# Performance work log

Hardware: AMD Instinct MI355X
Metric: run time of the kernel (lower is better)

Reference implementation:

```python
import jax, jax.numpy as jnp
import numpy as np

NUM_EXPERTS = 4


def _conv1x1(w, b, x):
    # w: [out,in], b: [out], x: [B,in,H,W]
    return jnp.einsum('oc,bchw->bohw', w, x) + b[None, :, None, None]


def _sobel(x):
    c = x.shape[1]
    kx = jnp.array([[-1., 0., 1.], [-2., 0., 2.], [-1., 0., 1.]], dtype=x.dtype)
    ky = jnp.array([[-1., -2., -1.], [0., 0., 0.], [1., 2., 1.]], dtype=x.dtype)
    wx = jnp.broadcast_to(kx[None, None], (c, 1, 3, 3))
    wy = jnp.broadcast_to(ky[None, None], (c, 1, 3, 3))
    dn = ('NCHW', 'OIHW', 'NCHW')
    gx = jax.lax.conv_general_dilated(x, wx, (1, 1), [(1, 1), (1, 1)],
                                      dimension_numbers=dn, feature_group_count=c)
    gy = jax.lax.conv_general_dilated(x, wy, (1, 1), [(1, 1), (1, 1)],
                                      dimension_numbers=dn, feature_group_count=c)
    return gx, gy


def _bilinear_sample(x, gx, gy):
    # torch F.grid_sample(mode='bilinear', padding_mode='zeros', align_corners=False)
    # x: [B,C,H,W]; gx, gy: [B,Hs,Ws] normalized coords in [-1,1]
    B, C, H, W = x.shape
    ix = ((gx + 1.0) * W - 1.0) * 0.5
    iy = ((gy + 1.0) * H - 1.0) * 0.5
    x0 = jnp.floor(ix)
    y0 = jnp.floor(iy)
    wx1 = ix - x0
    wx0 = 1.0 - wx1
    wy1 = iy - y0
    wy0 = 1.0 - wy1
    xf = x.reshape(B, C, H * W)

    def gather(xc, yc):
        valid = (xc >= 0) & (xc <= W - 1) & (yc >= 0) & (yc <= H - 1)
        xi = jnp.clip(xc, 0, W - 1).astype(jnp.int32)
        yi = jnp.clip(yc, 0, H - 1).astype(jnp.int32)
        idx = yi * W + xi  # [B,Hs,Ws]
        v = jax.vmap(lambda xb, ib: xb[:, ib])(xf, idx)  # [B,C,Hs,Ws]
        return v * valid[:, None].astype(x.dtype)

    return (gather(x0, y0) * (wx0 * wy0)[:, None]
            + gather(x0 + 1, y0) * (wx1 * wy0)[:, None]
            + gather(x0, y0 + 1) * (wx0 * wy1)[:, None]
            + gather(x0 + 1, y0 + 1) * (wx1 * wy1)[:, None])


def _forward(x, wc_e, we_e, wb1, bb1, wb2, bb2, wr, br, wo, bo, wcv, bcv, scale, scale2):
    B, c, h, w = x.shape
    sh = round(h * scale)
    sw = round(w * scale2)

    grad_x, grad_y = _sobel(x)

    # relative-offset coordinate embedding, [1,4,sh,sw]
    ih = (jnp.arange(sh, dtype=x.dtype) + 0.5) / scale
    coor_h = ih - jnp.floor(ih + 0.001) - 0.5  # [sh]
    iw = (jnp.arange(sw, dtype=x.dtype) + 0.5) / scale2
    coor_w = iw - jnp.floor(iw + 0.001) - 0.5  # [sw]
    inp = jnp.stack([
        jnp.full((sh, sw), 1.0 / scale2, dtype=x.dtype),
        jnp.full((sh, sw), 1.0 / scale, dtype=x.dtype),
        jnp.broadcast_to(coor_h[:, None], (sh, sw)),
        jnp.broadcast_to(coor_w[None, :], (sh, sw)),
    ], axis=0)[None]

    emb = jax.nn.relu(_conv1x1(wb2, bb2, jax.nn.relu(_conv1x1(wb1, bb1, inp))))
    offset = _conv1x1(wo, bo, emb)                 # [1,2,sh,sw]
    routing = jax.nn.sigmoid(_conv1x1(wr, br, emb))  # [1,E,sh,sw]

    # per-pixel soft mixture of expert compress/expand matrices
    rw = routing.reshape(NUM_EXPERTS, sh * sw).T   # [N,E]
    wc = (rw @ wc_e.reshape(NUM_EXPERTS, -1)).reshape(sh, sw, c // 8, c)
    we = (rw @ we_e.reshape(NUM_EXPERTS, -1)).reshape(sh, sw, c, c // 8)

    feat = _conv1x1(wcv, bcv, jnp.concatenate([x, grad_x, grad_y], axis=1))  # [B,64,h,w]

    # base grid (align_corners=True-style normalization, as in the source) + learned offsets
    gx0 = ((jnp.arange(sw, dtype=x.dtype) + 0.5) / scale2 - 0.5) * 2.0 / (w - 1) - 1.0
    gy0 = ((jnp.arange(sh, dtype=x.dtype) + 0.5) / scale - 0.5) * 2.0 / (h - 1) - 1.0
    gx = jnp.broadcast_to(gx0[None, None, :] + offset[:, 0] * (2.0 / (w - 1)), (B, sh, sw))
    gy = jnp.broadcast_to(gy0[None, :, None] + offset[:, 1] * (2.0 / (h - 1)), (B, sh, sw))

    fea0 = _bilinear_sample(feat, gx, gy)          # [B,64,sh,sw]

    mid = jnp.einsum('hwkc,bchw->bhwk', wc, fea0)  # per-pixel compress (k=C//8)
    out = jnp.einsum('hwck,bhwk->bchw', we, mid)   # per-pixel expand
    return out + fea0


def setup_inputs() -> dict:
    key = jax.random.key(0)
    ks = jax.random.split(key, 13)
    s = 0.05
    return {
        'x': jax.random.normal(ks[0], (2, 64, 192, 192), jnp.float32),
        'weight_compress': jax.random.normal(ks[1], (4, 8, 64), jnp.float32) * s,
        'weight_expand': jax.random.normal(ks[2], (4, 64, 8), jnp.float32) * s,
        'w_body1': jax.random.normal(ks[3], (64, 4), jnp.float32) * s,
        'b_body1': jax.random.normal(ks[4], (64,), jnp.float32) * s,
        'w_body2': jax.random.normal(ks[5], (64, 64), jnp.float32) * s,
        'b_body2': jax.random.normal(ks[6], (64,), jnp.float32) * s,
        'w_routing': jax.random.normal(ks[7], (4, 64), jnp.float32) * s,
        'b_routing': jax.random.normal(ks[8], (4,), jnp.float32) * s,
        'w_offset': jax.random.normal(ks[9], (2, 64), jnp.float32) * s,
        'b_offset': jax.random.normal(ks[10], (2,), jnp.float32) * s,
        'w_conv': jax.random.normal(ks[11], (64, 192), jnp.float32) * s,
        'b_conv': jax.random.normal(ks[12], (64,), jnp.float32) * s,
        'scale': 2,
        'scale2': 2,
    }


def reference(x, weight_compress, weight_expand, w_body1, b_body1, w_body2, b_body2,
              w_routing, b_routing, w_offset, b_offset, w_conv, b_conv, scale, scale2):
    return _forward(x, weight_compress, weight_expand, w_body1, b_body1, w_body2, b_body2,
                    w_routing, b_routing, w_offset, b_offset, w_conv, b_conv, scale, scale2)
```

## Files before the change

kernel.cpp:

```cpp
#include <hip/hip_runtime.h>
#include <hip/hip_bf16.h>
#include <math.h>

#define BN  2
#define CN  64
#define HN  192
#define WN  192
#define SH  384
#define SW  384
#define HW  (HN * WN)
#define NPIX (BN * HN * WN)

typedef __attribute__((ext_vector_type(8))) short bf16x8;
typedef __attribute__((ext_vector_type(4))) float f32x4;

#define CPAD  72
#define TRB   (BN * HN * 3)
#define TBLB  64

__device__ inline unsigned short f2bf(float f) {
    unsigned int u = __float_as_uint(f);
    u += 0x7fffu + ((u >> 16) & 1u);
    return (unsigned short)(u >> 16);
}
__device__ inline unsigned int pkbf(float a, float b) {
    return (unsigned int)f2bf(a) | ((unsigned int)f2bf(b) << 16);
}

__device__ inline void run_mlp(int lane, float in0, float in1, float chv, float cwv,
    const float* __restrict__ wb1, const float* __restrict__ bb1,
    const float* __restrict__ wb2, const float* __restrict__ bb2,
    const float* __restrict__ wr,  const float* __restrict__ wo, float p[6])
{
    float4 w1 = ((const float4*)wb1)[lane];
    float h1 = fmaxf(bb1[lane] + w1.x * in0 + w1.y * in1 + w1.z * chv + w1.w * cwv, 0.f);
    const float4* w2row = (const float4*)(wb2 + lane * 64);
    float acc = bb2[lane];
#pragma unroll
    for (int q = 0; q < 16; ++q) {
        float4 wv = w2row[q];
        acc += wv.x * __shfl(h1, q * 4 + 0)
             + wv.y * __shfl(h1, q * 4 + 1)
             + wv.z * __shfl(h1, q * 4 + 2)
             + wv.w * __shfl(h1, q * 4 + 3);
    }
    float h2 = fmaxf(acc, 0.f);
#pragma unroll
    for (int e = 0; e < 4; ++e) p[e] = wr[e * 64 + lane] * h2;
#pragma unroll
    for (int e = 0; e < 2; ++e) p[4 + e] = wo[e * 64 + lane] * h2;
#pragma unroll
    for (int m = 1; m < 64; m <<= 1) {
#pragma unroll
        for (int e = 0; e < 6; ++e) p[e] += __shfl_xor(p[e], m);
    }
}

__global__ __launch_bounds__(256) void prepass_kernel(
    const float* __restrict__ x,
    const float* __restrict__ wcv,
    const float* __restrict__ wb1, const float* __restrict__ bb1,
    const float* __restrict__ wb2, const float* __restrict__ bb2,
    const float* __restrict__ wr,  const float* __restrict__ br,
    const float* __restrict__ wo,  const float* __restrict__ bo,
    const float* __restrict__ wce, const float* __restrict__ wee,
    const int* __restrict__ scale_p, const int* __restrict__ scale2_p,
    unsigned short* __restrict__ xt,
    unsigned short* __restrict__ tblW,
    float* __restrict__ tblEntry, unsigned short* __restrict__ tblM)
{
    __shared__ __attribute__((aligned(16))) unsigned short sm[64 * CPAD];

    int tid  = threadIdx.x;
    int lane = tid & 63;
    int bi = blockIdx.x;

    if (bi < TRB) {
        int jt = bi % 3;
        int t2 = bi / 3;
        int i  = t2 % HN;
        int b  = t2 / HN;
        int j0 = jt * 64;
        int w  = tid >> 6;
        int c0 = w * 16;

        const float* xp = x + (size_t)b * CN * HW + (size_t)i * WN + j0 + lane;
#pragma unroll
        for (int k = 0; k < 16; k += 2) {
            float f0 = xp[(size_t)(c0 + k) * HW];
            float f1 = xp[(size_t)(c0 + k + 1) * HW];
            *(unsigned int*)(sm + lane * CPAD + c0 + k) = pkbf(f0, f1);
        }
        __syncthreads();
        size_t obase = (((size_t)b * HN + i) * WN + j0) * 64;
#pragma unroll
        for (int it = 0; it < 2; ++it) {
            int task = tid + it * 256;
            int jj = task >> 3, oc = task & 7;
            uint4 v = *(const uint4*)(sm + jj * CPAD + oc * 8);
            *(uint4*)(xt + obase + (size_t)jj * 64 + oc * 8) = v;
        }
        return;
    }

    if (bi == TRB) {
        const float KXc[9] = {-1.f, 0.f, 1.f, -2.f, 0.f, 2.f, -1.f, 0.f, 1.f};
        const float KYc[9] = {-1.f, -2.f, -1.f, 0.f, 0.f, 0.f, 1.f, 2.f, 1.f};
        int wv = tid >> 6;
        int o  = (wv << 4) + (lane & 15);
        const float* wp = wcv + o * 192;
        float v0[2][8], v1[2][8], v2[2][8];
#pragma unroll
        for (int kc = 0; kc < 2; ++kc) {
            int kb = kc * 32 + (lane >> 4) * 8;
            float4 a0 = *(const float4*)(wp + kb);
            float4 a1 = *(const float4*)(wp + kb + 4);
            float4 b0 = *(const float4*)(wp + 64 + kb);
            float4 b1 = *(const float4*)(wp + 64 + kb + 4);
            float4 c0 = *(const float4*)(wp + 128 + kb);
            float4 c1 = *(const float4*)(wp + 128 + kb + 4);
            v0[kc][0]=a0.x; v0[kc][1]=a0.y; v0[kc][2]=a0.z; v0[kc][3]=a0.w;
            v0[kc][4]=a1.x; v0[kc][5]=a1.y; v0[kc][6]=a1.z; v0[kc][7]=a1.w;
            v1[kc][0]=b0.x; v1[kc][1]=b0.y; v1[kc][2]=b0.z; v1[kc][3]=b0.w;
            v1[kc][4]=b1.x; v1[kc][5]=b1.y; v1[kc][6]=b1.z; v1[kc][7]=b1.w;
            v2[kc][0]=c0.x; v2[kc][1]=c0.y; v2[kc][2]=c0.z; v2[kc][3]=c0.w;
            v2[kc][4]=c1.x; v2[kc][5]=c1.y; v2[kc][6]=c1.z; v2[kc][7]=c1.w;
        }
#pragma unroll
        for (int t = 0; t < 9; ++t) {
#pragma unroll
            for (int kc = 0; kc < 2; ++kc) {
                bf16x8 a;
#pragma unroll
                for (int e = 0; e < 8; ++e) {
                    float f = v1[kc][e] * KXc[t] + v2[kc][e] * KYc[t];
                    if (t == 4) f += v0[kc][e];
                    a[e] = (short)f2bf(f);
                }
                *(bf16x8*)(void*)(tblW + (size_t)(((wv * 9 + t) * 2 + kc) * 64 + lane) * 8) = a;
            }
        }
        return;
    }

    {
        float* wcmL = (float*)sm;
        float* wemL = wcmL + 1024;
        float* reL  = wemL + 1024;

        int sc = scale_p[0], sc2 = scale2_p[0];
        float scale = (float)sc, scale2 = (float)sc2;
        float in0 = 1.f / scale2, in1 = 1.f / scale;
        bool fast = (sc2 == 2 && sc <= 16);
        int tb = bi - (TRB + 1);

        if (fast) {
            int pi = tb;
            if (pi >= sc) return;
            if (tid < 64) {
                float ih = (pi + 0.5f) / scale;
                float chv = ih - floorf(ih + 0.001f) - 0.5f;
                float p0[6], p1[6];
                {
                    float iw = 0.5f / scale2;
                    float cwv = iw - floorf(iw + 0.001f) - 0.5f;
                    run_mlp(lane, in0, in1, chv, cwv, wb1, bb1, wb2, bb2, wr, wo, p0);
                }
                {
                    float iw = 1.5f / scale2;
                    float cwv = iw - floorf(iw + 0.001f) - 0.5f;
                    run_mlp(lane, in0, in1, chv, cwv, wb1, bb1, wb2, bb2, wr, wo, p1);
                }
                if (lane == 0) {
                    float* t0 = tblEntry + (pi * 2 + 0) * 8;
                    float* t1 = tblEntry + (pi * 2 + 1) * 8;
#pragma unroll
                    for (int e = 0; e < 4; ++e) {
                        float rE = 1.f / (1.f + expf(-(p0[e] + br[e])));
                        float rO = 1.f / (1.f + expf(-(p1[e] + br[e])));
                        t0[e] = rE; t1[e] = rO;
                        reL[e] = rE; reL[4 + e] = rO;
                    }
                    t0[4] = p0[4] + bo[0]; t0[5] = p0[5] + bo[1];
                    t1[4] = p1[4] + bo[0]; t1[5] = p1[5] + bo[1];
                }
            }
            __syncthreads();
            float reE0 = reL[0], reE1 = reL[1], reE2 = reL[2], reE3 = reL[3];
            float reO0 = reL[4], reO1 = reL[5], reO2 = reL[6], reO3 = reL[7];
            for (int idx = tid; idx < 512; idx += 256) {
                float a = wce[idx], bq = wce[512 + idx], c = wce[1024 + idx], d = wce[1536 + idx];
                wcmL[idx]       = reE0 * a + reE1 * bq + reE2 * c + reE3 * d;
                wcmL[512 + idx] = reO0 * a + reO1 * bq + reO2 * c + reO3 * d;
                float e_ = wee[idx], f = wee[512 + idx], g = wee[1024 + idx], h = wee[1536 + idx];
                wemL[idx]       = reE0 * e_ + reE1 * f + reE2 * g + reE3 * h;
                wemL[512 + idx] = reO0 * e_ + reO1 * f + reO2 * g + reO3 * h;
            }
            __syncthreads();
            int co  = tid >> 2;
            int ci0 = (tid & 3) << 4;
            float w0[8], w1[8];
#pragma unroll
            for (int k = 0; k < 8; ++k) {
                w0[k] = wemL[co * 8 + k];
                w1[k] = wemL[512 + co * 8 + k];
            }
            unsigned short* tbp = tblM + (size_t)pi * 2 * 4096;
#pragma unroll
            for (int cc = 0; cc < 16; ++cc) {
                int ci = ci0 + cc;
                float m0 = 0.f, m1 = 0.f;
#pragma unroll
                for (int k = 0; k < 8; ++k) {
                    m0 += w0[k] * wcmL[k * 64 + ci];
                    m1 += w1[k] * wcmL[512 + k * 64 + ci];
                }
                tbp[co * 64 + ci]        = f2bf(0.5f * (m0 + m1));
                tbp[4096 + co * 64 + ci] = f2bf(0.5f * (m0 - m1));
            }
        } else {
            int w_ = (tb * 256 + tid) >> 6;
            if (w_ >= sc * sc2) return;
            int pi = w_ / sc2, pj = w_ - pi * sc2;
            float ih = (pi + 0.5f) / scale;
            float chv = ih - floorf(ih + 0.001f) - 0.5f;
            float iw = (pj + 0.5f) / scale2;
            float cwv = iw - floorf(iw + 0.001f) - 0.5f;
            float p[6];
            run_mlp(lane, in0, in1, chv, cwv, wb1, bb1, wb2, bb2, wr, wo, p);
            if (lane == 0) {
                float* tp = tblEntry + w_ * 8;
#pragma unroll
                for (int e = 0; e < 4; ++e) tp[e] = 1.f / (1.f + expf(-(p[e] + br[e])));
                tp[4] = p[4] + bo[0];
                tp[5] = p[5] + bo[1];
            }
        }
    }
}

__global__ __launch_bounds__(256) void feat_kernel(
    const unsigned short* __restrict__ xt,
    const unsigned short* __restrict__ tblW,
    const float* __restrict__ bcv,
    float* __restrict__ feat)
{
    __shared__ __attribute__((aligned(16))) unsigned short sm[198 * CPAD];

    int tid  = threadIdx.x;
    int lane = tid & 63;
    int bi = blockIdx.x;
    int jt = bi % 3;
    int t2 = bi / 3;
    int i0 = t2 % HN;
    int b  = t2 / HN;
    int j0 = jt * 64;
    int w  = __builtin_amdgcn_readfirstlane(tid >> 6);

    int row = lane & 15;
    int q   = lane >> 4;

    bf16x8 afrag[9][2];
#pragma unroll
    for (int t = 0; t < 9; ++t)
#pragma unroll
        for (int kc = 0; kc < 2; ++kc)
            afrag[t][kc] = *(const bf16x8*)(void*)(
                tblW + (size_t)(((w * 9 + t) * 2 + kc) * 64 + lane) * 8);

#pragma unroll
    for (int it = 0; it < 7; ++it) {
        int task = tid + it * 256;
        if (task < 198 * 8) {
            int p  = task >> 3;
            int oc = task & 7;
            int rowi = p / 66;
            int col  = p - rowi * 66;
            int sr = i0 - 1 + rowi;
            int hc = j0 - 1 + col;
            bool ok = (sr >= 0) && (sr < HN) && (hc >= 0) && (hc < WN);
            int srb = ok ? sr : 0;
            int hcb = ok ? hc : 0;
            uint4 v = *(const uint4*)(xt + (((size_t)b * HN + srb) * WN + hcb) * 64 + oc * 8);
            if (!ok) v = (uint4){0u, 0u, 0u, 0u};
            *(uint4*)(sm + p * CPAD + oc * 8) = v;
        }
    }

    __syncthreads();

    f32x4 acc[4] = {};
    const unsigned short* bb0 = sm + row * CPAD + (q << 3);
#pragma unroll
    for (int nt = 0; nt < 4; ++nt) {
#pragma unroll
        for (int t = 0; t < 9; ++t) {
            int a_ = t / 3, dxi = t - a_ * 3;
#pragma unroll
            for (int kc = 0; kc < 2; ++kc) {
                bf16x8 bv = *(const bf16x8*)(bb0 + (a_ * 66 + nt * 16 + dxi) * CPAD + kc * 32);
                acc[nt] = __builtin_amdgcn_mfma_f32_16x16x32_bf16(afrag[t][kc], bv, acc[nt], 0, 0, 0);
            }
        }
    }

    size_t rb0 = (size_t)b * CN * HW + (size_t)i0 * WN + j0 + row;
#pragma unroll
    for (int rr = 0; rr < 4; ++rr) {
        int oc = (w << 4) + q * 4 + rr;
        float bias = bcv[oc];
        size_t rowb = rb0 + (size_t)oc * HW;
#pragma unroll
        for (int nt = 0; nt < 4; ++nt)
            feat[rowb + nt * 16] = acc[nt][rr] + bias;
    }
}

#define BKP 72
__global__ __launch_bounds__(256) void out_kernel(
    const float* __restrict__ feat,
    const float* __restrict__ tblEntry,
    const unsigned short* __restrict__ tblM,
    const float* __restrict__ wce,
    const float* __restrict__ wee,
    const int* __restrict__ scale_p, const int* __restrict__ scale2_p,
    float* __restrict__ out)
{
    __shared__ __attribute__((aligned(16))) float smem[64 * 65 + 64 * (BKP / 2)];
    float* fea32 = smem;
    unsigned short* Bsv = (unsigned short*)(smem + 64 * 65);
    float* midp = smem;

    int Bk = blockIdx.x;
    int T = gridDim.x;
    int t = ((T & 7) == 0) ? ((Bk & 7) * (T >> 3) + (Bk >> 3)) : Bk;

    int tid = threadIdx.x;
    int g = __builtin_amdgcn_readfirstlane(tid >> 6);
    int lane = tid & 63;
    int pix0 = t * 64;
    int b = pix0 / (SH * SW);
    int r0 = pix0 - b * SH * SW;
    int i = r0 / SW;
    int j0 = r0 - i * SW;
    int j = j0 + lane;
    int r = r0 + lane;

    int sc = scale_p[0], sc2 = scale2_p[0];
    float scale = (float)sc, scale2 = (float)sc2;
    int pi = i - (i / sc) * sc;
    int pj = j - (j / sc2) * sc2;
    int entry = pi * sc2 + pj;
    float offx = tblEntry[entry * 8 + 4];
    float offy = tblEntry[entry * 8 + 5];

    const float inv_wm1 = 2.f / (float)(WN - 1);
    const float inv_hm1 = 2.f / (float)(HN - 1);
    float gx = ((j + 0.5f) / scale2 - 0.5f) * inv_wm1 - 1.f + offx * inv_wm1;
    float gy = ((i + 0.5f) / scale  - 0.5f) * inv_hm1 - 1.f + offy * inv_hm1;

    float ix = ((gx + 1.f) * WN - 1.f) * 0.5f;
    float iy = ((gy + 1.f) * HN - 1.f) * 0.5f;
    float fx0 = floorf(ix), fy0 = floorf(iy);
    int x0 = (int)fx0, y0 = (int)fy0;
    float wx1 = ix - fx0, wx0 = 1.f - wx1;
    float wy1 = iy - fy0, wy0 = 1.f - wy1;

    bool vx0 = (x0 >= 0) && (x0 <= WN - 1);
    bool vx1 = (x0 + 1 >= 0) && (x0 + 1 <= WN - 1);
    bool vy0 = (y0 >= 0) && (y0 <= HN - 1);
    bool vy1 = (y0 + 1 >= 0) && (y0 + 1 <= HN - 1);
    bool v00 = vx0 && vy0, v10 = vx1 && vy0, v01 = vx0 && vy1, v11 = vx1 && vy1;
    float w00 = wx0 * wy0, w10 = wx1 * wy0, w01 = wx0 * wy1, w11 = wx1 * wy1;

    int i00 = y0 * WN + x0;
    int i10 = i00 + 1;
    int i01 = i00 + WN;
    int i11 = i01 + 1;

    const float* fb = feat + (size_t)b * CN * HW;

    float f0[16];
#pragma unroll
    for (int cc = 0; cc < 16; ++cc) {
        const float* fc = fb + (size_t)(g * 16 + cc) * HW;
        float a  = v00 ? fc[i00] : 0.f;
        float bq = v10 ? fc[i10] : 0.f;
        float cq = v01 ? fc[i01] : 0.f;
        float dq = v11 ? fc[i11] : 0.f;
        f0[cc] = a * w00 + bq * w10 + cq * w01 + dq * w11;
    }

    bool fast = (sc2 == 2 && sc <= 16);
    if (fast) {
        int px = lane;
#pragma unroll
        for (int cc = 0; cc < 16; ++cc)
            fea32[px * 65 + g * 16 + cc] = f0[cc];
#pragma unroll
        for (int cc = 0; cc < 16; cc += 2) {
            unsigned int pk = (unsigned int)f2bf(f0[cc]) | ((unsigned int)f2bf(f0[cc + 1]) << 16);
            *(unsigned int*)(Bsv + px * BKP + g * 16 + cc) = pk;
        }

        int row = lane & 15;
        int kb  = (lane >> 4) << 3;
        const unsigned short* Mb = tblM + (size_t)pi * 2 * 4096 + (g * 16 + row) * 64 + kb;
        bf16x8 a1[2], a2[2];
        a1[0] = *(const bf16x8*)(Mb);
        a1[1] = *(const bf16x8*)(Mb + 32);
        a2[0] = *(const bf16x8*)(Mb + 4096);
        a2[1] = *(const bf16x8*)(Mb + 4096 + 32);

        __syncthreads();

        f32x4 acc1[4] = {}, acc2[4] = {};
        const unsigned short* bp = Bsv + (lane & 15) * BKP + kb;
#pragma unroll
        for (int nt = 0; nt < 4; ++nt) {
            const unsigned short* bnt = bp + nt * 16 * BKP;
#pragma unroll
            for (int ks = 0; ks < 2; ++ks) {
                bf16x8 bf = *(const bf16x8*)(bnt + ks * 32);
                acc1[nt] = __builtin_amdgcn_mfma_f32_16x16x32_bf16(a1[ks], bf, acc1[nt], 0, 0, 0);
                acc2[nt] = __builtin_amdgcn_mfma_f32_16x16x32_bf16(a2[ks], bf, acc2[nt], 0, 0, 0);
            }
        }

        int q = lane >> 4;
#pragma unroll
        for (int rr = 0; rr < 4; ++rr) {
            int c = g * 16 + q * 4 + rr;
            size_t rowb = (size_t)(b * CN + c) * SH * SW + r0;
#pragma unroll
            for (int nt = 0; nt < 4; ++nt) {
                int n = (lane & 15) + nt * 16;
                float sgn = (n & 1) ? -1.f : 1.f;
                float v = fea32[n * 65 + c] + acc1[nt][rr] + sgn * acc2[nt][rr];
                out[rowb + n] = v;
            }
        }
    } else {
        float4 rw = *(const float4*)(tblEntry + entry * 8);
        float re[4] = {rw.x, rw.y, rw.z, rw.w};
        float part[4][8];
#pragma unroll
        for (int e = 0; e < 4; ++e) {
#pragma unroll
            for (int k = 0; k < 8; ++k) {
                const float* wrow = wce + (e * 8 + k) * 64 + g * 16;
                float d = 0.f;
#pragma unroll
                for (int cc = 0; cc < 16; ++cc) d += wrow[cc] * f0[cc];
                part[e][k] = d;
            }
        }
#pragma unroll
        for (int k = 0; k < 8; ++k) {
            float m = re[0] * part[0][k] + re[1] * part[1][k]
                    + re[2] * part[2][k] + re[3] * part[3][k];
            midp[(g * 64 + lane) * 9 + k] = m;
        }
        __syncthreads();
        float mid[8];
#pragma unroll
        for (int k = 0; k < 8; ++k)
            mid[k] = midp[(0 * 64 + lane) * 9 + k] + midp[(1 * 64 + lane) * 9 + k]
                   + midp[(2 * 64 + lane) * 9 + k] + midp[(3 * 64 + lane) * 9 + k];
#pragma unroll
        for (int cc = 0; cc < 16; ++cc) {
            int c = g * 16 + cc;
            float v = f0[cc];
#pragma unroll
            for (int e = 0; e < 4; ++e) {
                const float* wrow = wee + (e * 64 + c) * 8;
                float d = 0.f;
#pragma unroll
                for (int k = 0; k < 8; ++k) d += wrow[k] * mid[k];
                v += re[e] * d;
            }
            out[(size_t)(b * CN + c) * SH * SW + r] = v;
        }
    }
}

extern "C" void kernel_launch(void* const* d_in, const int* in_sizes, int n_in,
                              void* d_out, int out_size, void* d_ws, size_t ws_size,
                              hipStream_t stream) {
    const float* x    = (const float*)d_in[0];
    const float* wce  = (const float*)d_in[1];
    const float* wee  = (const float*)d_in[2];
    const float* wb1  = (const float*)d_in[3];
    const float* bb1  = (const float*)d_in[4];
    const float* wb2  = (const float*)d_in[5];
    const float* bb2  = (const float*)d_in[6];
    const float* wr   = (const float*)d_in[7];
    const float* br   = (const float*)d_in[8];
    const float* wo   = (const float*)d_in[9];
    const float* bo   = (const float*)d_in[10];
    const float* wcv  = (const float*)d_in[11];
    const float* bcv  = (const float*)d_in[12];
    const int*   scale  = (const int*)d_in[13];
    const int*   scale2 = (const int*)d_in[14];
    float* out = (float*)d_out;

    float* feat     = (float*)d_ws;
    float* tblEntry = feat + (size_t)BN * CN * HW;
    unsigned short* tblM = (unsigned short*)(tblEntry + 2048);
    unsigned short* tblW = tblM + 16 * 2 * 4096;
    unsigned short* xt   = tblW + 4 * 9 * 2 * 64 * 8;

    prepass_kernel<<<TRB + 1 + TBLB, 256, 0, stream>>>(
        x, wcv, wb1, bb1, wb2, bb2, wr, br, wo, bo,
        wce, wee, scale, scale2, xt, tblW, tblEntry, tblM);
    feat_kernel<<<TRB, 256, 0, stream>>>(xt, tblW, bcv, feat);
    out_kernel<<<BN * SH * SW / 64, 256, 0, stream>>>(feat, tblEntry, tblM,
                                                      wce, wee, scale, scale2, out);
}
```

Baseline: 155.3 us.

## Store intermediate features as NHWC bf16 and vectorize bilinear gathers

The conv feature map is now written as channel-last bf16, staged through shared memory so each pixel's 64 channels are stored contiguously with 16-byte writes. The sampling kernel computes the four corner indices and weights once per pixel into shared memory, then gathers 8 channels per 16-byte load instead of scattered fp32 loads across channel planes. This halves intermediate traffic and makes the gathers coalesced, at the cost of rounding the intermediate features to bf16 and adding extra barriers.

```diff
diff --git a/kernel.cpp b/kernel.cpp
--- a/kernel.cpp
+++ b/kernel.cpp
@@ -25,6 +25,9 @@
 }
 __device__ inline unsigned int pkbf(float a, float b) {
     return (unsigned int)f2bf(a) | ((unsigned int)f2bf(b) << 16);
+}
+__device__ inline float bf2f(unsigned short u) {
+    return __uint_as_float((unsigned int)u << 16);
 }
 
 __device__ inline void run_mlp(int lane, float in0, float in1, float chv, float cwv,
@@ -243,7 +246,7 @@
     const unsigned short* __restrict__ xt,
     const unsigned short* __restrict__ tblW,
     const float* __restrict__ bcv,
-    float* __restrict__ feat)
+    unsigned short* __restrict__ featN)
 {
     __shared__ __attribute__((aligned(16))) unsigned short sm[198 * CPAD];
 
@@ -304,21 +307,36 @@
         }
     }
 
-    size_t rb0 = (size_t)b * CN * HW + (size_t)i0 * WN + j0 + row;
-#pragma unroll
-    for (int rr = 0; rr < 4; ++rr) {
-        int oc = (w << 4) + q * 4 + rr;
-        float bias = bcv[oc];
-        size_t rowb = rb0 + (size_t)oc * HW;
-#pragma unroll
-        for (int nt = 0; nt < 4; ++nt)
-            feat[rowb + nt * 16] = acc[nt][rr] + bias;
+    __syncthreads();
+    {
+        int oc0 = (w << 4) + (q << 2);
+        float b0 = bcv[oc0], b1 = bcv[oc0 + 1], b2 = bcv[oc0 + 2], b3 = bcv[oc0 + 3];
+#pragma unroll
+        for (int nt = 0; nt < 4; ++nt) {
+            int px = nt * 16 + row;
+            uint2 uu;
+            uu.x = pkbf(acc[nt][0] + b0, acc[nt][1] + b1);
+            uu.y = pkbf(acc[nt][2] + b2, acc[nt][3] + b3);
+            *(uint2*)(sm + px * CPAD + oc0) = uu;
+        }
+    }
+    __syncthreads();
+    {
+        size_t obase = ((size_t)b * HN + i0) * WN + j0;
+#pragma unroll
+        for (int it = 0; it < 2; ++it) {
+            int task = tid + it * 256;
+            int px = task >> 3, oc = task & 7;
+            uint4 v = *(const uint4*)(sm + px * CPAD + oc * 8);
+            *(uint4*)(featN + (obase + px) * 64 + oc * 8) = v;
+        }
     }
 }
 
 #define BKP 72
+#define FPAD 68
 __global__ __launch_bounds__(256) void out_kernel(
-    const float* __restrict__ feat,
+    const unsigned short* __restrict__ featN,
     const float* __restrict__ tblEntry,
     const unsigned short* __restrict__ tblM,
     const float* __restrict__ wce,
@@ -326,10 +344,11 @@
     const int* __restrict__ scale_p, const int* __restrict__ scale2_p,
     float* __restrict__ out)
 {
-    __shared__ __attribute__((aligned(16))) float smem[64 * 65 + 64 * (BKP / 2)];
-    float* fea32 = smem;
-    unsigned short* Bsv = (unsigned short*)(smem + 64 * 65);
-    float* midp = smem;
+    __shared__ __attribute__((aligned(16))) float fea32[64 * FPAD];
+    __shared__ __attribute__((aligned(16))) unsigned short Bsv[64 * BKP];
+    __shared__ int   cidx[4 * 64];
+    __shared__ float cwt[4 * 64];
+    float* midp = fea32;
 
     int Bk = blockIdx.x;
     int T = gridDim.x;
@@ -343,64 +362,46 @@
     int r0 = pix0 - b * SH * SW;
     int i = r0 / SW;
     int j0 = r0 - i * SW;
-    int j = j0 + lane;
-    int r = r0 + lane;
 
     int sc = scale_p[0], sc2 = scale2_p[0];
     float scale = (float)sc, scale2 = (float)sc2;
     int pi = i - (i / sc) * sc;
-    int pj = j - (j / sc2) * sc2;
-    int entry = pi * sc2 + pj;
-    float offx = tblEntry[entry * 8 + 4];
-    float offy = tblEntry[entry * 8 + 5];
-
     const float inv_wm1 = 2.f / (float)(WN - 1);
     const float inv_hm1 = 2.f / (float)(HN - 1);
-    float gx = ((j + 0.5f) / scale2 - 0.5f) * inv_wm1 - 1.f + offx * inv_wm1;
-    float gy = ((i + 0.5f) / scale  - 0.5f) * inv_hm1 - 1.f + offy * inv_hm1;
-
-    float ix = ((gx + 1.f) * WN - 1.f) * 0.5f;
-    float iy = ((gy + 1.f) * HN - 1.f) * 0.5f;
-    float fx0 = floorf(ix), fy0 = floorf(iy);
-    int x0 = (int)fx0, y0 = (int)fy0;
-    float wx1 = ix - fx0, wx0 = 1.f - wx1;
-    float wy1 = iy - fy0, wy0 = 1.f - wy1;
-
-    bool vx0 = (x0 >= 0) && (x0 <= WN - 1);
-    bool vx1 = (x0 + 1 >= 0) && (x0 + 1 <= WN - 1);
-    bool vy0 = (y0 >= 0) && (y0 <= HN - 1);
-    bool vy1 = (y0 + 1 >= 0) && (y0 + 1 <= HN - 1);
-    bool v00 = vx0 && vy0, v10 = vx1 && vy0, v01 = vx0 && vy1, v11 = vx1 && vy1;
-    float w00 = wx0 * wy0, w10 = wx1 * wy0, w01 = wx0 * wy1, w11 = wx1 * wy1;
-
-    int i00 = y0 * WN + x0;
-    int i10 = i00 + 1;
-    int i01 = i00 + WN;
-    int i11 = i01 + 1;
-
-    const float* fb = feat + (size_t)b * CN * HW;
-
-    float f0[16];
-#pragma unroll
-    for (int cc = 0; cc < 16; ++cc) {
-        const float* fc = fb + (size_t)(g * 16 + cc) * HW;
-        float a  = v00 ? fc[i00] : 0.f;
-        float bq = v10 ? fc[i10] : 0.f;
-        float cq = v01 ? fc[i01] : 0.f;
-        float dq = v11 ? fc[i11] : 0.f;
-        f0[cc] = a * w00 + bq * w10 + cq * w01 + dq * w11;
-    }
 
     bool fast = (sc2 == 2 && sc <= 16);
     if (fast) {
-        int px = lane;
-#pragma unroll
-        for (int cc = 0; cc < 16; ++cc)
-            fea32[px * 65 + g * 16 + cc] = f0[cc];
-#pragma unroll
-        for (int cc = 0; cc < 16; cc += 2) {
-            unsigned int pk = (unsigned int)f2bf(f0[cc]) | ((unsigned int)f2bf(f0[cc + 1]) << 16);
-            *(unsigned int*)(Bsv + px * BKP + g * 16 + cc) = pk;
+        if (tid < 64) {
+            int px = tid;
+            int jpx = j0 + px;
+            int pjx = jpx - (jpx / sc2) * sc2;
+            int entry = pi * sc2 + pjx;
+            float offx = tblEntry[entry * 8 + 4];
+            float offy = tblEntry[entry * 8 + 5];
+            float gx = ((jpx + 0.5f) / scale2 - 0.5f) * inv_wm1 - 1.f + offx * inv_wm1;
+            float gy = ((i + 0.5f) / scale  - 0.5f) * inv_hm1 - 1.f + offy * inv_hm1;
+            float ix = ((gx + 1.f) * WN - 1.f) * 0.5f;
+            float iy = ((gy + 1.f) * HN - 1.f) * 0.5f;
+            float fx0 = floorf(ix), fy0 = floorf(iy);
+            int x0 = (int)fx0, y0 = (int)fy0;
+            float wx1 = ix - fx0, wx0 = 1.f - wx1;
+            float wy1 = iy - fy0, wy0 = 1.f - wy1;
+            bool vx0 = (x0 >= 0) && (x0 <= WN - 1);
+            bool vx1 = (x0 + 1 >= 0) && (x0 + 1 <= WN - 1);
+            bool vy0 = (y0 >= 0) && (y0 <= HN - 1);
+            bool vy1 = (y0 + 1 >= 0) && (y0 + 1 <= HN - 1);
+            int x0c = min(max(x0, 0), WN - 1);
+            int x1c = min(max(x0 + 1, 0), WN - 1);
+            int y0c = min(max(y0, 0), HN - 1);
+            int y1c = min(max(y0 + 1, 0), HN - 1);
+            cidx[0 * 64 + px] = y0c * WN + x0c;
+            cidx[1 * 64 + px] = y0c * WN + x1c;
+            cidx[2 * 64 + px] = y1c * WN + x0c;
+            cidx[3 * 64 + px] = y1c * WN + x1c;
+            cwt[0 * 64 + px] = wx0 * wy0 * ((vx0 && vy0) ? 1.f : 0.f);
+            cwt[1 * 64 + px] = wx1 * wy0 * ((vx1 && vy0) ? 1.f : 0.f);
+            cwt[2 * 64 + px] = wx0 * wy1 * ((vx0 && vy1) ? 1.f : 0.f);
+            cwt[3 * 64 + px] = wx1 * wy1 * ((vx1 && vy1) ? 1.f : 0.f);
         }
 
         int row = lane & 15;
@@ -414,6 +415,35 @@
 
         __syncthreads();
 
+        const unsigned short* fb = featN + (size_t)b * HW * 64;
+#pragma unroll
+        for (int it = 0; it < 2; ++it) {
+            int task = tid + it * 256;
+            int px = task >> 3, oct = task & 7;
+            const unsigned short* fo = fb + oct * 8;
+            float a8[8] = {};
+#pragma unroll
+            for (int k = 0; k < 4; ++k) {
+                bf16x8 cv = *(const bf16x8*)(fo + (size_t)cidx[k * 64 + px] * 64);
+                float wk = cwt[k * 64 + px];
+#pragma unroll
+                for (int e = 0; e < 8; ++e)
+                    a8[e] += wk * bf2f((unsigned short)cv[e]);
+            }
+            float4 lo = {a8[0], a8[1], a8[2], a8[3]};
+            float4 hi = {a8[4], a8[5], a8[6], a8[7]};
+            *(float4*)(fea32 + px * FPAD + oct * 8)     = lo;
+            *(float4*)(fea32 + px * FPAD + oct * 8 + 4) = hi;
+            uint4 pk;
+            pk.x = pkbf(a8[0], a8[1]);
+            pk.y = pkbf(a8[2], a8[3]);
+            pk.z = pkbf(a8[4], a8[5]);
+            pk.w = pkbf(a8[6], a8[7]);
+            *(uint4*)(Bsv + px * BKP + oct * 8) = pk;
+        }
+
+        __syncthreads();
+
         f32x4 acc1[4] = {}, acc2[4] = {};
         const unsigned short* bp = Bsv + (lane & 15) * BKP + kb;
 #pragma unroll
@@ -436,11 +466,51 @@
             for (int nt = 0; nt < 4; ++nt) {
                 int n = (lane & 15) + nt * 16;
                 float sgn = (n & 1) ? -1.f : 1.f;
-                float v = fea32[n * 65 + c] + acc1[nt][rr] + sgn * acc2[nt][rr];
+                float v = fea32[n * FPAD + c] + acc1[nt][rr] + sgn * acc2[nt][rr];
                 out[rowb + n] = v;
             }
         }
     } else {
+        int j = j0 + lane;
+        int r = r0 + lane;
+        int pj = j - (j / sc2) * sc2;
+        int entry = pi * sc2 + pj;
+        float offx = tblEntry[entry * 8 + 4];
+        float offy = tblEntry[entry * 8 + 5];
+        float gx = ((j + 0.5f) / scale2 - 0.5f) * inv_wm1 - 1.f + offx * inv_wm1;
+        float gy = ((i + 0.5f) / scale  - 0.5f) * inv_hm1 - 1.f + offy * inv_hm1;
+        float ix = ((gx + 1.f) * WN - 1.f) * 0.5f;
+        float iy = ((gy + 1.f) * HN - 1.f) * 0.5f;
+        float fx0 = floorf(ix), fy0 = floorf(iy);
+        int x0 = (int)fx0, y0 = (int)fy0;
+        float wx1 = ix - fx0, wx0 = 1.f - wx1;
+        float wy1 = iy - fy0, wy0 = 1.f - wy1;
+        bool vx0 = (x0 >= 0) && (x0 <= WN - 1);
+        bool vx1 = (x0 + 1 >= 0) && (x0 + 1 <= WN - 1);
+        bool vy0 = (y0 >= 0) && (y0 <= HN - 1);
+        bool vy1 = (y0 + 1 >= 0) && (y0 + 1 <= HN - 1);
+        int x0c = min(max(x0, 0), WN - 1);
+        int x1c = min(max(x0 + 1, 0), WN - 1);
+        int y0c = min(max(y0, 0), HN - 1);
+        int y1c = min(max(y0 + 1, 0), HN - 1);
+        float w00 = wx0 * wy0 * ((vx0 && vy0) ? 1.f : 0.f);
+        float w10 = wx1 * wy0 * ((vx1 && vy0) ? 1.f : 0.f);
+        float w01 = wx0 * wy1 * ((vx0 && vy1) ? 1.f : 0.f);
+        float w11 = wx1 * wy1 * ((vx1 && vy1) ? 1.f : 0.f);
+        const unsigned short* fb = featN + ((size_t)b * HW) * 64;
+        const unsigned short* p00 = fb + (size_t)(y0c * WN + x0c) * 64;
+        const unsigned short* p10 = fb + (size_t)(y0c * WN + x1c) * 64;
+        const unsigned short* p01 = fb + (size_t)(y1c * WN + x0c) * 64;
+        const unsigned short* p11 = fb + (size_t)(y1c * WN + x1c) * 64;
+
+        float f0[16];
+#pragma unroll
+        for (int cc = 0; cc < 16; ++cc) {
+            int c = g * 16 + cc;
+            f0[cc] = bf2f(p00[c]) * w00 + bf2f(p10[c]) * w10
+                   + bf2f(p01[c]) * w01 + bf2f(p11[c]) * w11;
+        }
+
         float4 rw = *(const float4*)(tblEntry + entry * 8);
         float re[4] = {rw.x, rw.y, rw.z, rw.w};
         float part[4][8];
@@ -504,16 +574,16 @@
     const int*   scale2 = (const int*)d_in[14];
     float* out = (float*)d_out;
 
-    float* feat     = (float*)d_ws;
-    float* tblEntry = feat + (size_t)BN * CN * HW;
-    unsigned short* tblM = (unsigned short*)(tblEntry + 2048);
+    unsigned short* featN = (unsigned short*)d_ws;
+    float* tblEntry = (float*)((char*)d_ws + (size_t)BN * HW * 64 * 2);
+    unsigned short* tblM = (unsigned short*)((char*)tblEntry + 2048 * 4);
     unsigned short* tblW = tblM + 16 * 2 * 4096;
     unsigned short* xt   = tblW + 4 * 9 * 2 * 64 * 8;
 
     prepass_kernel<<<TRB + 1 + TBLB, 256, 0, stream>>>(
         x, wcv, wb1, bb1, wb2, bb2, wr, br, wo, bo,
         wce, wee, scale, scale2, xt, tblW, tblEntry, tblM);
-    feat_kernel<<<TRB, 256, 0, stream>>>(xt, tblW, bcv, feat);
-    out_kernel<<<BN * SH * SW / 64, 256, 0, stream>>>(feat, tblEntry, tblM,
+    feat_kernel<<<TRB, 256, 0, stream>>>(xt, tblW, bcv, featN);
+    out_kernel<<<BN * SH * SW / 64, 256, 0, stream>>>(featN, tblEntry, tblM,
                                                       wce, wee, scale, scale2, out);
 }
```

Result: no change. 152.6 us (-1.7%).
